# Performance work log

Measured on AMD Instinct MI355X. Metric: run time of the kernel, lower is better.

## Reference

```python
import jax, jax.numpy as jnp
import numpy as np

N_NODES = 40000
N_EDGES = 640000
D = 128
BN_EPS = 1e-5
GATE_EPS = 1e-6


def _linear_params(key, d_in, d_out):
    kw, kb = jax.random.split(key)
    bound = 1.0 / np.sqrt(d_in)
    W = jax.random.uniform(kw, (d_out, d_in), jnp.float32, -bound, bound)
    b = jax.random.uniform(kb, (d_out,), jnp.float32, -bound, bound)
    return W, b


def setup_inputs() -> dict:
    key = jax.random.key(0)
    ks = jax.random.split(key, 8)
    x = jax.random.normal(ks[0], (N_NODES, D), jnp.float32)
    edge_index = jax.random.randint(ks[1], (2, N_EDGES), 0, N_NODES, jnp.int64)
    edge_attr = jax.random.normal(ks[2], (N_EDGES, D), jnp.float32)
    W_src_gate, b_src_gate = _linear_params(ks[3], D, D)
    W_dst_gate, b_dst_gate = _linear_params(ks[4], D, D)
    W_edge_gate, b_edge_gate = _linear_params(ks[5], D, D)
    W_src_update, b_src_update = _linear_params(ks[6], D, D)
    W_dst_update, b_dst_update = _linear_params(ks[7], D, D)
    return dict(
        x=x, edge_index=edge_index, edge_attr=edge_attr,
        W_src_gate=W_src_gate, b_src_gate=b_src_gate,
        W_dst_gate=W_dst_gate, b_dst_gate=b_dst_gate,
        W_edge_gate=W_edge_gate, b_edge_gate=b_edge_gate,
        W_src_update=W_src_update, b_src_update=b_src_update,
        W_dst_update=W_dst_update, b_dst_update=b_dst_update,
        bn_nodes_gamma=jnp.ones((D,), jnp.float32), bn_nodes_beta=jnp.zeros((D,), jnp.float32),
        bn_edges_gamma=jnp.ones((D,), jnp.float32), bn_edges_beta=jnp.zeros((D,), jnp.float32),
    )


def _batch_norm(z, gamma, beta):
    # training-mode BN: batch mean, biased variance (torch semantics)
    mean = jnp.mean(z, axis=0)
    var = jnp.mean(jnp.square(z - mean), axis=0)
    return gamma * (z - mean) * jax.lax.rsqrt(var + BN_EPS) + beta


def reference(x, edge_index, edge_attr,
              W_src_gate, b_src_gate, W_dst_gate, b_dst_gate,
              W_edge_gate, b_edge_gate, W_src_update, b_src_update,
              W_dst_update, b_dst_update,
              bn_nodes_gamma, bn_nodes_beta, bn_edges_gamma, bn_edges_beta):
    row, col = edge_index[0], edge_index[1]
    num_nodes = x.shape[0]
    x_row = x[row]                      # [E, D] gather
    x_col = x[col]                      # [E, D] gather
    e_src = x_row @ W_src_gate.T + b_src_gate
    e_dst = x_col @ W_dst_gate.T + b_dst_gate
    m = e_src + e_dst + edge_attr @ W_edge_gate.T + b_edge_gate  # [E, D]
    sigma = jax.nn.sigmoid(m)
    h_weighted = (x_col @ W_dst_update.T + b_dst_update) * sigma
    h_sum = jax.ops.segment_sum(h_weighted, col, num_segments=num_nodes)
    sigma_sum = jax.ops.segment_sum(sigma, col, num_segments=num_nodes)
    h_normalized = h_sum / (sigma_sum + GATE_EPS)
    x_new = x @ W_src_update.T + b_src_update + h_normalized
    x_new = jax.nn.softplus(_batch_norm(x_new, bn_nodes_gamma, bn_nodes_beta))
    y_new = jax.nn.softplus(_batch_norm(m, bn_edges_gamma, bn_edges_beta))
    x_new = x + x_new          # residual
    y_new = edge_attr + y_new  # residual
    return (x_new, y_new)
```

## Files before the change

### kernel.cpp

```cpp
#include <hip/hip_runtime.h>

#define NN 40000
#define NE 640000

typedef unsigned short u16;
typedef unsigned int u32;
typedef __attribute__((ext_vector_type(4))) float f32x4;
typedef __attribute__((ext_vector_type(8))) __bf16 bf16x8;

#define LSTR 132
#define TPW 8

__device__ __forceinline__ float bf2f(u16 u) { return __uint_as_float(((u32)u) << 16); }
__device__ __forceinline__ u16 f2bf(float f) {
  u32 u = __float_as_uint(f);
  u32 r = 0x7fffu + ((u >> 16) & 1u);
  return (u16)((u + r) >> 16);
}
__device__ __forceinline__ float splus(float v) {
  return fmaxf(v, 0.0f) + __logf(1.0f + __expf(-fabsf(v)));
}

__global__ void sniff_k(const u32* __restrict__ gamma, const u32* __restrict__ eidx,
                        u32* __restrict__ flags) {
  if (threadIdx.x == 0) {
    flags[0] = (gamma[0] == 0x3F803F80u) ? 1u : 0u;
    u32 odd = eidx[1] | eidx[3] | eidx[5] | eidx[7] |
              eidx[9] | eidx[11] | eidx[13] | eidx[15];
    flags[1] = (odd == 0u) ? 1u : 0u;
  }
}

__device__ __forceinline__ int load_col(const void* eidx, int e, u32 i64) {
  int nc = i64 ? (int)((const u32*)eidx)[2 * ((size_t)NE + e)]
               : ((const int*)eidx)[NE + e];
  return min(max(nc, 0), NN - 1);
}
__device__ __forceinline__ int load_row(const void* eidx, int e, u32 i64) {
  int nr = i64 ? (int)((const u32*)eidx)[2 * (size_t)e]
               : ((const int*)eidx)[e];
  return min(max(nr, 0), NN - 1);
}

__global__ __launch_bounds__(256) void wconv5_k(
    const float* __restrict__ W0, const float* __restrict__ W1,
    const float* __restrict__ W2, const float* __restrict__ W3,
    const float* __restrict__ W4, u16* __restrict__ out) {
  int i = blockIdx.x * 256 + threadIdx.x;
  int mtx = blockIdx.y;
  const float* W = (mtx == 0) ? W0 : (mtx == 1) ? W1 : (mtx == 2) ? W2
                 : (mtx == 3) ? W3 : W4;
  out[mtx * 16384 + i] = f2bf(W[i]);
}

__global__ __launch_bounds__(256) void hist_k(const void* __restrict__ eidx,
                                              u32* __restrict__ cnt,
                                              const u32* __restrict__ flags) {
  int e = blockIdx.x * 256 + threadIdx.x;
  atomicAdd(&cnt[load_col(eidx, e, flags[1])], 1u);
}

__device__ __forceinline__ bf16x8 a_frag(const float* __restrict__ row, int kbase) {
  float4 f0 = *(const float4*)(row + kbase);
  float4 f1 = *(const float4*)(row + kbase + 4);
  bf16x8 a;
  a[0] = (__bf16)f0.x; a[1] = (__bf16)f0.y; a[2] = (__bf16)f0.z; a[3] = (__bf16)f0.w;
  a[4] = (__bf16)f1.x; a[5] = (__bf16)f1.y; a[6] = (__bf16)f1.z; a[7] = (__bf16)f1.w;
  return a;
}

__device__ __forceinline__ bf16x8 cvt8(float4 a, float4 b) {
  bf16x8 r;
  r[0] = (__bf16)a.x; r[1] = (__bf16)a.y; r[2] = (__bf16)a.z; r[3] = (__bf16)a.w;
  r[4] = (__bf16)b.x; r[5] = (__bf16)b.y; r[6] = (__bf16)b.z; r[7] = (__bf16)b.w;
  return r;
}

__device__ __forceinline__ void gemm16(const bf16x8 af[4], const u16* __restrict__ Wb,
                                       const float* __restrict__ bias, int lane,
                                       f32x4 acc[8]) {
  int l15 = lane & 15, lk = lane >> 4;
#pragma unroll
  for (int n = 0; n < 8; ++n) {
    float bv = bias[n * 16 + l15];
    acc[n] = (f32x4){bv, bv, bv, bv};
  }
#pragma unroll
  for (int n = 0; n < 8; ++n) {
    const u16* bp = Wb + (size_t)(n * 16 + l15) * 128 + lk * 8;
#pragma unroll
    for (int k = 0; k < 4; ++k) {
      bf16x8 b = *(const bf16x8*)(bp + 32 * k);
      acc[n] = __builtin_amdgcn_mfma_f32_16x16x32_bf16(af[k], b, acc[n], 0, 0, 0);
    }
  }
}

__device__ __forceinline__ void store_tile(u16* __restrict__ out, int m0, int lane,
                                           const f32x4 acc[8]) {
  int l15 = lane & 15, lk = lane >> 4;
#pragma unroll
  for (int n = 0; n < 8; ++n)
#pragma unroll
    for (int r = 0; r < 4; ++r)
      out[(size_t)(m0 + lk * 4 + r) * 128 + n * 16 + l15] = f2bf(acc[n][r]);
}

__global__ __launch_bounds__(256) void node_gemm_k(
    const float* __restrict__ x, const u16* __restrict__ Wb,
    const float* __restrict__ B0, const float* __restrict__ B1,
    const float* __restrict__ B2, const float* __restrict__ B3,
    const u32* __restrict__ cnt,
    u16* __restrict__ o0, u16* __restrict__ o1,
    u16* __restrict__ o2, u16* __restrict__ o3,
    float* __restrict__ statsg) {
  __shared__ float red[256];
  int tid = threadIdx.x, lane = tid & 63, w = tid >> 6;
  for (int i = tid; i < 256; i += 256) red[i] = 0.f;
  __syncthreads();
  int m0 = blockIdx.x * 64 + w * 16;
  int l15 = lane & 15, lk = lane >> 4;
  const float* arow = x + (size_t)(m0 + l15) * 128;
  bf16x8 af[4];
#pragma unroll
  for (int k = 0; k < 4; ++k) af[k] = a_frag(arow, 32 * k + 8 * lk);
  f32x4 acc[8], accd[8];
  gemm16(af, Wb + 0 * 16384, B0, lane, acc);  store_tile(o0, m0, lane, acc);
  gemm16(af, Wb + 1 * 16384, B1, lane, acc);  store_tile(o1, m0, lane, acc);
  gemm16(af, Wb + 2 * 16384, B2, lane, accd); store_tile(o2, m0, lane, accd);
  gemm16(af, Wb + 3 * 16384, B3, lane, acc);  store_tile(o3, m0, lane, acc);
  float g[4];
#pragma unroll
  for (int r = 0; r < 4; ++r) g[r] = (cnt[m0 + lk * 4 + r] != 0u) ? 1.0f : 0.0f;
#pragma unroll
  for (int n = 0; n < 8; ++n) {
    float a1 = 0.f, a2 = 0.f;
#pragma unroll
    for (int r = 0; r < 4; ++r) {
      float zv = acc[n][r] + g[r] * accd[n][r];
      a1 += zv;
      a2 = fmaf(zv, zv, a2);
    }
    a1 += __shfl_xor(a1, 16); a1 += __shfl_xor(a1, 32);
    a2 += __shfl_xor(a2, 16); a2 += __shfl_xor(a2, 32);
    if (lk == 0) {
      atomicAdd(&red[n * 16 + l15], a1);
      atomicAdd(&red[128 + n * 16 + l15], a2);
    }
  }
  __syncthreads();
  for (int i = tid; i < 256; i += 256) atomicAdd(&statsg[256 + i], red[i]);
}

__global__ __launch_bounds__(256, 2) void edge_gemm_k(
    const float* __restrict__ ea, const u16* __restrict__ Wgb,
    const float* __restrict__ Bg,
    const u16* __restrict__ g_src, const u16* __restrict__ g_dst,
    const void* __restrict__ eidx,
    u16* __restrict__ mge, float* __restrict__ statsg,
    const u32* __restrict__ flags) {
  __shared__ __align__(16) u16 mt[4][16][LSTR];
  __shared__ __align__(16) float gt[4][16][LSTR];
  int tid = threadIdx.x, lane = tid & 63, w = tid >> 6;
  int l15 = lane & 15, lk = lane >> 4;
  u32 i64 = flags[1];

  bf16x8 bf[8][4];
#pragma unroll
  for (int n = 0; n < 8; ++n)
#pragma unroll
    for (int k = 0; k < 4; ++k)
      bf[n][k] = *(const bf16x8*)(Wgb + (size_t)(n * 16 + l15) * 128 + lk * 8 + 32 * k);
  float bias[8];
#pragma unroll
  for (int n = 0; n < 8; ++n) bias[n] = Bg[n * 16 + l15];

  float e1[8] = {0.f, 0.f, 0.f, 0.f, 0.f, 0.f, 0.f, 0.f};
  float e2[8] = {0.f, 0.f, 0.f, 0.f, 0.f, 0.f, 0.f, 0.f};

  int base = (blockIdx.x * 4 + w) * (TPW * 16);
  const float* aptr = ea + (size_t)(base + l15) * 128 + 8 * lk;

  float4 tmp[8];
#pragma unroll
  for (int k = 0; k < 4; ++k) {
    tmp[2 * k]     = *(const float4*)(aptr + 32 * k);
    tmp[2 * k + 1] = *(const float4*)(aptr + 32 * k + 4);
  }
  bf16x8 af[4];
#pragma unroll
  for (int k = 0; k < 4; ++k) af[k] = cvt8(tmp[2 * k], tmp[2 * k + 1]);

  for (int t = 0; t < TPW; ++t) {
    int e0 = base + t * 16;
    int eg = e0 + (lane >> 2);
    int grow = load_row(eidx, eg, i64);
    int gcol = load_col(eidx, eg, i64);
#pragma unroll
    for (int it = 0; it < 4; ++it) {
      int ch = (lane & 3) + 4 * it;
      uint4 gsv = *(const uint4*)(g_src + (size_t)grow * 128 + ch * 8);
      uint4 gdv = *(const uint4*)(g_dst + (size_t)gcol * 128 + ch * 8);
      const u16* sp = (const u16*)&gsv;
      const u16* dp = (const u16*)&gdv;
      float4 lo, hi;
      lo.x = bf2f(sp[0]) + bf2f(dp[0]);
      lo.y = bf2f(sp[1]) + bf2f(dp[1]);
      lo.z = bf2f(sp[2]) + bf2f(dp[2]);
      lo.w = bf2f(sp[3]) + bf2f(dp[3]);
      hi.x = bf2f(sp[4]) + bf2f(dp[4]);
      hi.y = bf2f(sp[5]) + bf2f(dp[5]);
      hi.z = bf2f(sp[6]) + bf2f(dp[6]);
      hi.w = bf2f(sp[7]) + bf2f(dp[7]);
      *(float4*)&gt[w][lane >> 2][ch * 8]     = lo;
      *(float4*)&gt[w][lane >> 2][ch * 8 + 4] = hi;
    }
    if (t + 1 < TPW) {
      const float* anx = aptr + (size_t)(t + 1) * 16 * 128;
#pragma unroll
      for (int k = 0; k < 4; ++k) {
        tmp[2 * k]     = *(const float4*)(anx + 32 * k);
        tmp[2 * k + 1] = *(const float4*)(anx + 32 * k + 4);
      }
    }
    f32x4 acc[8];
#pragma unroll
    for (int n = 0; n < 8; ++n)
      acc[n] = (f32x4){bias[n], bias[n], bias[n], bias[n]};
#pragma unroll
    for (int n = 0; n < 8; ++n)
#pragma unroll
      for (int k = 0; k < 4; ++k)
        acc[n] = __builtin_amdgcn_mfma_f32_16x16x32_bf16(af[k], bf[n][k], acc[n], 0, 0, 0);
#pragma unroll
    for (int n = 0; n < 8; ++n) {
#pragma unroll
      for (int r = 0; r < 4; ++r) {
        float mv = acc[n][r] + gt[w][lk * 4 + r][n * 16 + l15];
        e1[n] += mv;
        e2[n] = fmaf(mv, mv, e2[n]);
        mt[w][lk * 4 + r][n * 16 + l15] = f2bf(mv);
      }
    }
    if (t + 1 < TPW) {
#pragma unroll
      for (int k = 0; k < 4; ++k) af[k] = cvt8(tmp[2 * k], tmp[2 * k + 1]);
    }
#pragma unroll
    for (int it = 0; it < 4; ++it) {
      int row = lane >> 2, ch = (lane & 3) + 4 * it;
      uint4 v = *(const uint4*)&mt[w][row][ch * 8];
      *(uint4*)(mge + (size_t)(e0 + row) * 128 + ch * 8) = v;
    }
  }
#pragma unroll
  for (int n = 0; n < 8; ++n) {
    float s1 = e1[n], s2 = e2[n];
    s1 += __shfl_xor(s1, 16); s1 += __shfl_xor(s1, 32);
    s2 += __shfl_xor(s2, 16); s2 += __shfl_xor(s2, 32);
    if (lk == 0) {
      atomicAdd(&statsg[n * 16 + l15], s1);
      atomicAdd(&statsg[128 + n * 16 + l15], s2);
    }
  }
}

__global__ void stats_fin_k(const float* __restrict__ es1, const float* __restrict__ es2,
                            const float* __restrict__ ns1, const float* __restrict__ ns2,
                            const float* __restrict__ eg_, const float* __restrict__ eb_,
                            const float* __restrict__ ng_, const float* __restrict__ nb_,
                            float* __restrict__ params) {
  int d = threadIdx.x;
  float em = es1[d] * (1.0f / NE);
  float ev = fmaxf(es2[d] * (1.0f / NE) - em * em, 0.0f);
  float esc = eg_[d] * rsqrtf(ev + 1e-5f);
  params[d] = esc;
  params[128 + d] = eb_[d] - em * esc;
  float nm = ns1[d] * (1.0f / NN);
  float nv = fmaxf(ns2[d] * (1.0f / NN) - nm * nm, 0.0f);
  float nsc = ng_[d] * rsqrtf(nv + 1e-5f);
  params[256 + d] = nsc;
  params[384 + d] = nb_[d] - nm * nsc;
}

__global__ __launch_bounds__(256) void node_fin2_k(
    const float* __restrict__ x, const u16* __restrict__ us,
    const u16* __restrict__ ud, const u32* __restrict__ cnt,
    const float* __restrict__ params, float* __restrict__ out) {
  size_t t = (size_t)blockIdx.x * 256 + threadIdx.x;
  size_t base = t * 8;
  int d0 = (int)(base & 127);
  int n = (int)(t >> 4);
  float g = (cnt[n] != 0u) ? 1.0f : 0.0f;
  float4 xa = *(const float4*)(x + base);
  float4 xb = *(const float4*)(x + base + 4);
  float xv[8] = {xa.x, xa.y, xa.z, xa.w, xb.x, xb.y, xb.z, xb.w};
  uint4 usv = *(const uint4*)(us + base);
  uint4 udv = *(const uint4*)(ud + base);
  const u16* up = (const u16*)&usv;
  const u16* dp = (const u16*)&udv;
  float o[8];
#pragma unroll
  for (int j = 0; j < 8; ++j) {
    float z = bf2f(up[j]) + g * bf2f(dp[j]);
    float bnv = z * params[256 + d0 + j] + params[384 + d0 + j];
    o[j] = xv[j] + splus(bnv);
  }
  *(float4*)(out + base) = make_float4(o[0], o[1], o[2], o[3]);
  *(float4*)(out + base + 4) = make_float4(o[4], o[5], o[6], o[7]);
}

__global__ __launch_bounds__(256) void edge_fin_k(
    const float* __restrict__ edge_attr, const u16* __restrict__ mge,
    const float* __restrict__ params, float* __restrict__ out) {
  size_t t = (size_t)blockIdx.x * 256 + threadIdx.x;
  size_t base = t * 8;
  int d0 = (int)(base & 127);
  float4 ea = *(const float4*)(edge_attr + base);
  float4 eb = *(const float4*)(edge_attr + base + 4);
  float ev[8] = {ea.x, ea.y, ea.z, ea.w, eb.x, eb.y, eb.z, eb.w};
  uint4 mv_ = *(const uint4*)(mge + base);
  const u16* mp = (const u16*)&mv_;
  float o[8];
#pragma unroll
  for (int j = 0; j < 8; ++j) {
    float m = bf2f(mp[j]);
    float bnv = m * params[d0 + j] + params[128 + d0 + j];
    o[j] = ev[j] + splus(bnv);
  }
  *(float4*)(out + base) = make_float4(o[0], o[1], o[2], o[3]);
  *(float4*)(out + base + 4) = make_float4(o[4], o[5], o[6], o[7]);
}

extern "C" void kernel_launch(void* const* d_in, const int* in_sizes, int n_in,
                              void* d_out, int out_size, void* d_ws, size_t ws_size,
                              hipStream_t stream) {
  const float* x        = (const float*)d_in[0];
  const void*  eidx     = d_in[1];
  const float* edge_att = (const float*)d_in[2];
  const float* Wsg = (const float*)d_in[3];  const float* bsg = (const float*)d_in[4];
  const float* Wdg = (const float*)d_in[5];  const float* bdg = (const float*)d_in[6];
  const float* Weg = (const float*)d_in[7];  const float* beg = (const float*)d_in[8];
  const float* Wsu = (const float*)d_in[9];  const float* bsu = (const float*)d_in[10];
  const float* Wdu = (const float*)d_in[11]; const float* bdu = (const float*)d_in[12];
  const float* bng = (const float*)d_in[13]; const float* bnb = (const float*)d_in[14];
  const float* beg_g = (const float*)d_in[15]; const float* beb = (const float*)d_in[16];

  char* ws = (char*)d_ws;
  u16*   g_src  = (u16*)(ws + 0);
  u16*   g_dst  = (u16*)(ws + 10240000);
  u16*   u_dst  = (u16*)(ws + 20480000);
  u16*   u_src  = (u16*)(ws + 30720000);
  float* stats  = (float*)(ws + 40960000);
  u32*   flags  = (u32*)(ws + 40964096);
  u16*   wbuf   = (u16*)(ws + 40968192);
  u32*   cnt    = (u32*)(ws + 41132032);
  u16*   mge    = (u16*)(ws + 41292032);

  hipMemsetAsync(stats, 0, 4096, stream);
  hipMemsetAsync(cnt, 0, 160000, stream);

  sniff_k<<<1, 64, 0, stream>>>((const u32*)bng, (const u32*)eidx, flags);
  wconv5_k<<<dim3(64, 5), 256, 0, stream>>>(Wsg, Wdg, Wdu, Wsu, Weg, wbuf);
  hist_k<<<NE / 256, 256, 0, stream>>>(eidx, cnt, flags);
  node_gemm_k<<<NN / 64, 256, 0, stream>>>(x, wbuf, bsg, bdg, bdu, bsu, cnt,
                                           g_src, g_dst, u_dst, u_src, stats);
  edge_gemm_k<<<NE / (64 * TPW), 256, 0, stream>>>(edge_att, wbuf + 4 * 16384, beg,
                                                   g_src, g_dst, eidx,
                                                   mge, stats, flags);
  stats_fin_k<<<1, 128, 0, stream>>>(stats, stats + 128, stats + 256, stats + 384,
                                     beg_g, beb, bng, bnb, stats + 512);
  node_fin2_k<<<(NN * 128) / 2048, 256, 0, stream>>>(x, u_src, u_dst, cnt,
                                                     stats + 512, (float*)d_out);
  edge_fin_k<<<(NE * 128) / 2048, 256, 0, stream>>>(edge_att, mge, stats + 512,
                                                    (float*)d_out + (size_t)NN * 128);
}
```

Before: 558.0 us.

## Software-pipeline edge gathers and index loads, use nontemporal streaming in edge GEMM

In the edge GEMM kernel, the gathered g_src/g_dst rows for the next tile are now loaded into registers one iteration ahead, and edge indices two iterations ahead, so gather latency overlaps the MFMA work. Streaming edge_attr reads and the mge writes use nontemporal loads and stores to reduce cache pollution. Tiles per wave drop from 8 to 4, which raises block count but shortens the pipeline and adds more per-block weight-loading overhead. The extra prefetch registers may raise register pressure under the 2-blocks-per-SM launch bound.

```diff
diff --git a/kernel.cpp b/kernel.cpp
--- a/kernel.cpp
+++ b/kernel.cpp
@@ -6,10 +6,12 @@
 typedef unsigned short u16;
 typedef unsigned int u32;
 typedef __attribute__((ext_vector_type(4))) float f32x4;
+typedef __attribute__((ext_vector_type(4))) float fv4;
+typedef __attribute__((ext_vector_type(4))) u32 uv4;
 typedef __attribute__((ext_vector_type(8))) __bf16 bf16x8;
 
 #define LSTR 132
-#define TPW 8
+#define TPW 4
 
 __device__ __forceinline__ float bf2f(u16 u) { return __uint_as_float(((u32)u) << 16); }
 __device__ __forceinline__ u16 f2bf(float f) {
@@ -19,6 +21,9 @@
 }
 __device__ __forceinline__ float splus(float v) {
   return fmaxf(v, 0.0f) + __logf(1.0f + __expf(-fabsf(v)));
+}
+__device__ __forceinline__ fv4 ntl4(const float* p) {
+  return __builtin_nontemporal_load((const fv4*)p);
 }
 
 __global__ void sniff_k(const u32* __restrict__ gamma, const u32* __restrict__ eidx,
@@ -69,10 +74,10 @@
   return a;
 }
 
-__device__ __forceinline__ bf16x8 cvt8(float4 a, float4 b) {
+__device__ __forceinline__ bf16x8 cvt8v(fv4 a, fv4 b) {
   bf16x8 r;
-  r[0] = (__bf16)a.x; r[1] = (__bf16)a.y; r[2] = (__bf16)a.z; r[3] = (__bf16)a.w;
-  r[4] = (__bf16)b.x; r[5] = (__bf16)b.y; r[6] = (__bf16)b.z; r[7] = (__bf16)b.w;
+  r[0] = (__bf16)a[0]; r[1] = (__bf16)a[1]; r[2] = (__bf16)a[2]; r[3] = (__bf16)a[3];
+  r[4] = (__bf16)b[0]; r[5] = (__bf16)b[1]; r[6] = (__bf16)b[2]; r[7] = (__bf16)b[3];
   return r;
 }
 
@@ -163,6 +168,7 @@
   __shared__ __align__(16) float gt[4][16][LSTR];
   int tid = threadIdx.x, lane = tid & 63, w = tid >> 6;
   int l15 = lane & 15, lk = lane >> 4;
+  int el = lane >> 2, c4 = lane & 3;
   u32 i64 = flags[1];
 
   bf16x8 bf[8][4];
@@ -181,47 +187,59 @@
   int base = (blockIdx.x * 4 + w) * (TPW * 16);
   const float* aptr = ea + (size_t)(base + l15) * 128 + 8 * lk;
 
-  float4 tmp[8];
+  int rowc = load_row(eidx, base + el, i64);
+  int colc = load_col(eidx, base + el, i64);
+  uv4 gsv[4], gdv[4];
+#pragma unroll
+  for (int it = 0; it < 4; ++it) {
+    gsv[it] = *(const uv4*)(g_src + (size_t)rowc * 128 + c4 * 8 + it * 32);
+    gdv[it] = *(const uv4*)(g_dst + (size_t)colc * 128 + c4 * 8 + it * 32);
+  }
+  fv4 tmp[8];
 #pragma unroll
   for (int k = 0; k < 4; ++k) {
-    tmp[2 * k]     = *(const float4*)(aptr + 32 * k);
-    tmp[2 * k + 1] = *(const float4*)(aptr + 32 * k + 4);
+    tmp[2 * k]     = ntl4(aptr + 32 * k);
+    tmp[2 * k + 1] = ntl4(aptr + 32 * k + 4);
   }
   bf16x8 af[4];
 #pragma unroll
-  for (int k = 0; k < 4; ++k) af[k] = cvt8(tmp[2 * k], tmp[2 * k + 1]);
+  for (int k = 0; k < 4; ++k) af[k] = cvt8v(tmp[2 * k], tmp[2 * k + 1]);
+  int rown = load_row(eidx, base + 16 + el, i64);
+  int coln = load_col(eidx, base + 16 + el, i64);
 
   for (int t = 0; t < TPW; ++t) {
-    int e0 = base + t * 16;
-    int eg = e0 + (lane >> 2);
-    int grow = load_row(eidx, eg, i64);
-    int gcol = load_col(eidx, eg, i64);
 #pragma unroll
     for (int it = 0; it < 4; ++it) {
-      int ch = (lane & 3) + 4 * it;
-      uint4 gsv = *(const uint4*)(g_src + (size_t)grow * 128 + ch * 8);
-      uint4 gdv = *(const uint4*)(g_dst + (size_t)gcol * 128 + ch * 8);
-      const u16* sp = (const u16*)&gsv;
-      const u16* dp = (const u16*)&gdv;
-      float4 lo, hi;
-      lo.x = bf2f(sp[0]) + bf2f(dp[0]);
-      lo.y = bf2f(sp[1]) + bf2f(dp[1]);
-      lo.z = bf2f(sp[2]) + bf2f(dp[2]);
-      lo.w = bf2f(sp[3]) + bf2f(dp[3]);
-      hi.x = bf2f(sp[4]) + bf2f(dp[4]);
-      hi.y = bf2f(sp[5]) + bf2f(dp[5]);
-      hi.z = bf2f(sp[6]) + bf2f(dp[6]);
-      hi.w = bf2f(sp[7]) + bf2f(dp[7]);
-      *(float4*)&gt[w][lane >> 2][ch * 8]     = lo;
-      *(float4*)&gt[w][lane >> 2][ch * 8 + 4] = hi;
+      int ch = c4 + 4 * it;
+      const u16* sp = (const u16*)&gsv[it];
+      const u16* dp = (const u16*)&gdv[it];
+      fv4 lo, hi;
+#pragma unroll
+      for (int j = 0; j < 4; ++j) lo[j] = bf2f(sp[j]) + bf2f(dp[j]);
+#pragma unroll
+      for (int j = 0; j < 4; ++j) hi[j] = bf2f(sp[4 + j]) + bf2f(dp[4 + j]);
+      *(fv4*)&gt[w][el][ch * 8]     = lo;
+      *(fv4*)&gt[w][el][ch * 8 + 4] = hi;
     }
     if (t + 1 < TPW) {
       const float* anx = aptr + (size_t)(t + 1) * 16 * 128;
 #pragma unroll
       for (int k = 0; k < 4; ++k) {
-        tmp[2 * k]     = *(const float4*)(anx + 32 * k);
-        tmp[2 * k + 1] = *(const float4*)(anx + 32 * k + 4);
+        tmp[2 * k]     = ntl4(anx + 32 * k);
+        tmp[2 * k + 1] = ntl4(anx + 32 * k + 4);
       }
+    }
+    if (t + 1 < TPW) {
+#pragma unroll
+      for (int it = 0; it < 4; ++it) {
+        gsv[it] = *(const uv4*)(g_src + (size_t)rown * 128 + c4 * 8 + it * 32);
+        gdv[it] = *(const uv4*)(g_dst + (size_t)coln * 128 + c4 * 8 + it * 32);
+      }
+    }
+    int rn2 = rown, cn2 = coln;
+    if (t + 2 < TPW) {
+      rn2 = load_row(eidx, base + (t + 2) * 16 + el, i64);
+      cn2 = load_col(eidx, base + (t + 2) * 16 + el, i64);
     }
     f32x4 acc[8];
 #pragma unroll
@@ -242,16 +260,18 @@
         mt[w][lk * 4 + r][n * 16 + l15] = f2bf(mv);
       }
     }
+    int e0 = base + t * 16;
+#pragma unroll
+    for (int it = 0; it < 4; ++it) {
+      int ch = c4 + 4 * it;
+      uv4 v = *(const uv4*)&mt[w][el][ch * 8];
+      __builtin_nontemporal_store(v, (uv4*)(mge + (size_t)(e0 + el) * 128 + ch * 8));
+    }
     if (t + 1 < TPW) {
 #pragma unroll
-      for (int k = 0; k < 4; ++k) af[k] = cvt8(tmp[2 * k], tmp[2 * k + 1]);
-    }
-#pragma unroll
-    for (int it = 0; it < 4; ++it) {
-      int row = lane >> 2, ch = (lane & 3) + 4 * it;
-      uint4 v = *(const uint4*)&mt[w][row][ch * 8];
-      *(uint4*)(mge + (size_t)(e0 + row) * 128 + ch * 8) = v;
-    }
+      for (int k = 0; k < 4; ++k) af[k] = cvt8v(tmp[2 * k], tmp[2 * k + 1]);
+    }
+    rown = rn2; coln = cn2;
   }
 #pragma unroll
   for (int n = 0; n < 8; ++n) {
```

New measurement: 583.6 us. +4.6%, slower.
